# Optimization experiments

Measured on AMD Instinct MI355X. Metric: run time of the kernel, lower is better.

## Reference

```python
import jax, jax.numpy as jnp
import numpy as np

EPS = 1e-5       # InstanceNorm1d default eps
TEMP = 1.0       # temperature
SCALE = 8
# (name, arity) of the symbolic base, repeated SCALE times -> 48 functions, layer_size = 64
BASE = [("add", 2), ("mul", 2), ("sin", 1), ("cos", 1), ("tanh", 1), ("identity", 1)]


def _apply(name, a):
    if name == "add":
        return a[0] + a[1]
    if name == "mul":
        return a[0] * a[1]
    if name == "sin":
        return jnp.sin(a[0])
    if name == "cos":
        return jnp.cos(a[0])
    if name == "tanh":
        return jnp.tanh(a[0])
    return a[0]  # identity


def _inorm(x):
    # InstanceNorm1d, affine=False, biased variance, per (sample, channel) over L
    m = jnp.mean(x, axis=-1, keepdims=True)
    v = jnp.var(x, axis=-1, keepdims=True)
    return (x - m) * jax.lax.rsqrt(v + EPS)


def setup_inputs() -> dict:
    key = jax.random.key(0)
    k1, k2, k3 = jax.random.split(key, 3)
    x = jax.random.normal(k1, (64, 256, 4096), dtype=jnp.float32)
    w_channel = 0.1 * jax.random.normal(k2, (64, 256), dtype=jnp.float32)   # channel_conv 1x1
    w_down = 0.1 * jax.random.normal(k3, (48, 256), dtype=jnp.float32)      # down_conv 1x1
    return {"x": x, "w_channel": w_channel, "w_down": w_down}


def reference(x, w_channel, w_down):
    funcs = BASE * SCALE
    nx = _inorm(x)                                   # [B, C, L]
    # forward softmaxes channel_conv weight over output-channel dim (dim=0)
    w_eff = jax.nn.softmax(w_channel / TEMP, axis=0)  # [layer_size, C]
    multi = jnp.einsum("oc,bcl->bol", w_eff, nx)      # [B, layer_size, L]
    args_idx = 0
    output = None
    for i, (name, arity) in enumerate(funcs):
        args = [multi[:, args_idx + j : args_idx + j + 1] for j in range(arity)]
        img = _apply(name, args)                      # [B, 1, L]
        output = img if i == 0 else jnp.concatenate([output, img], axis=1)
        # original re-applies InstanceNorm to the growing tensor each iteration
        output = _inorm(output)
        args_idx += arity
    # skip connection
    output = output + jnp.einsum("oc,bcl->bol", w_down, nx)  # [B, 48, L]
    return output
```

## Files before the change

### kernel.cpp

```cpp
#include <hip/hip_runtime.h>
#include <hip/hip_bf16.h>

#define EPS 1e-5f

typedef unsigned int u32;
typedef unsigned short u16;
typedef __attribute__((ext_vector_type(8))) short bf16x8;
typedef __attribute__((ext_vector_type(4))) float f32x4;

__device__ __forceinline__ u32 f2bf(float f) {
    u32 u = __float_as_uint(f);
    u += 0x7FFFu + ((u >> 16) & 1u);
    return u >> 16;
}
__device__ __forceinline__ float bf2f(u32 h) {
    return __uint_as_float(h << 16);
}

__global__ __launch_bounds__(256) void k1_stats(const float* __restrict__ x,
                                                float* __restrict__ mean,
                                                float* __restrict__ rstd) {
    int row = blockIdx.x;
    const float* xr = x + (size_t)row * 4096;
    int t = threadIdx.x;
    float s = 0.f, ss = 0.f;
#pragma unroll
    for (int i = 0; i < 4; ++i) {
        float4 v = *(const float4*)(xr + t * 4 + i * 1024);
        s  += v.x + v.y + v.z + v.w;
        ss += v.x * v.x + v.y * v.y + v.z * v.z + v.w * v.w;
    }
    for (int off = 32; off > 0; off >>= 1) {
        s  += __shfl_down(s, off, 64);
        ss += __shfl_down(ss, off, 64);
    }
    __shared__ float red[8];
    int wid = t >> 6, lane = t & 63;
    if (lane == 0) { red[wid * 2] = s; red[wid * 2 + 1] = ss; }
    __syncthreads();
    if (t == 0) {
        float S  = red[0] + red[2] + red[4] + red[6];
        float SS = red[1] + red[3] + red[5] + red[7];
        float m = S * (1.f / 4096.f);
        float v = fmaxf(SS * (1.f / 4096.f) - m * m, 0.f);
        mean[row] = m;
        rstd[row] = rsqrtf(v + EPS);
    }
}

__global__ __launch_bounds__(256) void k2_prep(const float* __restrict__ wch,
                                               const float* __restrict__ wdn,
                                               const float* __restrict__ mean,
                                               const float* __restrict__ rstd,
                                               u16* __restrict__ Wc,
                                               float* __restrict__ bias,
                                               float* __restrict__ gsum,
                                               float* __restrict__ gss) {
    int b = blockIdx.x, t = threadIdx.x;
    __shared__ float smx[256], sinv[256], ssc[256], smn[256];
    {
        int c = t;
        float mx = -1e30f;
        for (int o = 0; o < 64; ++o) mx = fmaxf(mx, wch[o * 256 + c]);
        float sum = 0.f;
        for (int o = 0; o < 64; ++o) sum += __expf(wch[o * 256 + c] - mx);
        smx[c] = mx; sinv[c] = 1.f / sum;
        ssc[c] = rstd[b * 256 + c];
        smn[c] = mean[b * 256 + c];
    }
    __syncthreads();

    int lane = t & 63, w = t >> 6;
    int sub = lane >> 5, li = lane & 31;
    int c8 = li * 8;
    u16* Wb = Wc + (size_t)b * 128 * 256;
#pragma unroll 4
    for (int j = 0; j < 16; ++j) {
        int r = j * 8 + w * 2 + sub;
        float p = 0.f;
        u32 packed[4];
#pragma unroll
        for (int e = 0; e < 4; ++e) {
            u32 lohi[2];
#pragma unroll
            for (int h = 0; h < 2; ++h) {
                int c = c8 + 2 * e + h;
                float wv;
                if (r < 64)       wv = __expf(wch[r * 256 + c] - smx[c]) * sinv[c];
                else if (r < 112) wv = wdn[(r - 64) * 256 + c];
                else              wv = 0.f;
                u32 hb = f2bf(wv * ssc[c]);
                lohi[h] = hb;
                p += bf2f(hb) * smn[c];
            }
            packed[e] = lohi[0] | (lohi[1] << 16);
        }
        *(uint4*)&Wb[r * 256 + c8] = *(uint4*)packed;
#pragma unroll
        for (int off = 1; off <= 16; off <<= 1) p += __shfl_xor(p, off, 64);
        if (li == 0) bias[b * 128 + r] = -p;
    }
    if (t < 48) { gsum[b * 48 + t] = 0.f; gss[b * 48 + t] = 0.f; }
}

#define LSTR 36
__global__ __launch_bounds__(256, 4) void k3_main(const float* __restrict__ x,
                                                  const u16* __restrict__ Wc,
                                                  const float* __restrict__ bias,
                                                  u16* __restrict__ imgw,
                                                  u16* __restrict__ skipw,
                                                  float* __restrict__ gsum,
                                                  float* __restrict__ gss) {
    int lt = blockIdx.x;
    int b  = blockIdx.y;
    int n0blk = lt * 128;
    int t = threadIdx.x;
    int w = t >> 6, u = t & 63;
    int lane16 = u & 15, q = u >> 4;
    int m0  = (w & 1) * 64;
    int n0w = (w >> 1) * 64;

    __shared__ u32 Wl[128 * LSTR];
    __shared__ u32 xTl[128 * LSTR];
    __shared__ float sbias[128];

    if (t < 128) sbias[t] = bias[b * 128 + t];

    f32x4 acc[4][4];
#pragma unroll
    for (int mt = 0; mt < 4; ++mt)
#pragma unroll
        for (int nt = 0; nt < 4; ++nt) acc[mt][nt] = (f32x4){0.f, 0.f, 0.f, 0.f};

    const float* xb = x + (size_t)b * 256 * 4096 + n0blk;
    const u16* Wb = Wc + (size_t)b * 128 * 256;

    for (int cc = 0; cc < 4; ++cc) {
        int c0 = cc * 64;
        if (cc) __syncthreads();
#pragma unroll
        for (int p = 0; p < 4; ++p) {
            int sl = t + 256 * p;
            int m = sl >> 3, kq = sl & 7;
            uint4 v = *(const uint4*)(Wb + m * 256 + c0 + 8 * kq);
            *(uint4*)&Wl[m * LSTR + 4 * kq] = v;
        }
#pragma unroll
        for (int p = 0; p < 4; ++p) {
            int sl = t + 256 * p;
            int kp = sl & 31, nqq = sl >> 5;
            const float* xr = xb + (size_t)(c0 + 2 * kp) * 4096 + 4 * nqq;
            float4 r0 = *(const float4*)xr;
            float4 r1 = *(const float4*)(xr + 4096);
            int base = (4 * nqq) * LSTR + kp;
            xTl[base]            = f2bf(r0.x) | (f2bf(r1.x) << 16);
            xTl[base + LSTR]     = f2bf(r0.y) | (f2bf(r1.y) << 16);
            xTl[base + 2 * LSTR] = f2bf(r0.z) | (f2bf(r1.z) << 16);
            xTl[base + 3 * LSTR] = f2bf(r0.w) | (f2bf(r1.w) << 16);
        }
        __syncthreads();
#pragma unroll
        for (int kk = 0; kk < 2; ++kk) {
            int kwo = kk * 16 + q * 4;
            bf16x8 af[4], bfr[4];
#pragma unroll
            for (int mt = 0; mt < 4; ++mt)
                af[mt] = *(bf16x8*)&Wl[(m0 + 16 * mt + lane16) * LSTR + kwo];
#pragma unroll
            for (int nt = 0; nt < 4; ++nt)
                bfr[nt] = *(bf16x8*)&xTl[(n0w + 16 * nt + lane16) * LSTR + kwo];
#pragma unroll
            for (int mt = 0; mt < 4; ++mt)
#pragma unroll
                for (int nt = 0; nt < 4; ++nt)
                    acc[mt][nt] = __builtin_amdgcn_mfma_f32_16x16x32_bf16(af[mt], bfr[nt], acc[mt][nt], 0, 0, 0);
        }
    }
    __syncthreads();

    int jb = b * 48;
    if (m0 == 0) {
        int g2 = q >> 1, qo = q & 1;
#pragma unroll
        for (int mt = 0; mt < 4; ++mt) {
            int g = 2 * mt + g2;
            int j0 = 6 * g + (qo ? 2 : 0);
            int cnt = qo ? 4 : 2;
            float b0 = sbias[16 * mt + 4 * q + 0];
            float b1 = sbias[16 * mt + 4 * q + 1];
            float b2 = sbias[16 * mt + 4 * q + 2];
            float b3 = sbias[16 * mt + 4 * q + 3];
            float sj[4] = {0.f, 0.f, 0.f, 0.f};
            float qj[4] = {0.f, 0.f, 0.f, 0.f};
#pragma unroll
            for (int nt = 0; nt < 4; ++nt) {
                f32x4 a = acc[mt][nt];
                float a0 = a[0] + b0, a1 = a[1] + b1, a2 = a[2] + b2, a3 = a[3] + b3;
                int n = n0blk + n0w + 16 * nt + lane16;
                float v[4];
                if (!qo) {
                    v[0] = a0 + a1;
                    v[1] = a2 * a3;
                    v[2] = 0.f; v[3] = 0.f;
                } else {
                    v[0] = __sinf(a0);
                    v[1] = __cosf(a1);
                    float e = __expf(-2.f * fabsf(a2));
                    v[2] = copysignf((1.f - e) / (1.f + e), a2);
                    v[3] = a3;
                }
                for (int i = 0; i < cnt; ++i) {
                    imgw[(size_t)(jb + j0 + i) * 4096 + n] = (u16)f2bf(v[i]);
                    sj[i] += v[i];
                    qj[i] += v[i] * v[i];
                }
            }
#pragma unroll
            for (int off = 1; off <= 8; off <<= 1) {
#pragma unroll
                for (int i = 0; i < 4; ++i) {
                    sj[i] += __shfl_xor(sj[i], off, 64);
                    qj[i] += __shfl_xor(qj[i], off, 64);
                }
            }
            if (lane16 == 0) {
                for (int i = 0; i < cnt; ++i) {
                    atomicAdd(&gsum[jb + j0 + i], sj[i]);
                    atomicAdd(&gss[jb + j0 + i],  qj[i]);
                }
            }
        }
    } else {
#pragma unroll
        for (int mt = 0; mt < 3; ++mt) {
            int j0 = 16 * mt + 4 * q;
            float b0 = sbias[64 + j0 + 0];
            float b1 = sbias[64 + j0 + 1];
            float b2 = sbias[64 + j0 + 2];
            float b3 = sbias[64 + j0 + 3];
#pragma unroll
            for (int nt = 0; nt < 4; ++nt) {
                f32x4 a = acc[mt][nt];
                int n = n0blk + n0w + 16 * nt + lane16;
                skipw[(size_t)(jb + j0 + 0) * 4096 + n] = (u16)f2bf(a[0] + b0);
                skipw[(size_t)(jb + j0 + 1) * 4096 + n] = (u16)f2bf(a[1] + b1);
                skipw[(size_t)(jb + j0 + 2) * 4096 + n] = (u16)f2bf(a[2] + b2);
                skipw[(size_t)(jb + j0 + 3) * 4096 + n] = (u16)f2bf(a[3] + b3);
            }
        }
    }
}

__global__ __launch_bounds__(256) void k4_final(const u16* __restrict__ imgw,
                                                const u16* __restrict__ skipw,
                                                const float* __restrict__ gsum,
                                                const float* __restrict__ gss,
                                                float* __restrict__ out) {
    int j = blockIdx.x, b = blockIdx.y;
    int bj = b * 48 + j;
    float m = gsum[bj] * (1.f / 4096.f);
    float v = fmaxf(gss[bj] * (1.f / 4096.f) - m * m, 0.f);
    float rs = rsqrtf(v + EPS);
    float g = 1.f;
    float vv = v / (v + EPS);
    for (int k = 0; k < 47 - j; ++k) {
        g *= rsqrtf(vv + EPS);
        vv = vv / (vv + EPS);
    }
    float sc = rs * g;
    const u16* ir = imgw  + (size_t)bj * 4096;
    const u16* sr = skipw + (size_t)bj * 4096;
    float* orow = out + (size_t)bj * 4096;
    int t = threadIdx.x;
#pragma unroll
    for (int i = 0; i < 2; ++i) {
        int idx = t * 8 + i * 2048;
        uint4 iv = *(const uint4*)(ir + idx);
        uint4 sv = *(const uint4*)(sr + idx);
        const u32* ih = (const u32*)&iv;
        const u32* sh = (const u32*)&sv;
        float o[8];
#pragma unroll
        for (int e = 0; e < 4; ++e) {
            float i_lo = bf2f(ih[e] & 0xFFFFu), i_hi = bf2f(ih[e] >> 16);
            float s_lo = bf2f(sh[e] & 0xFFFFu), s_hi = bf2f(sh[e] >> 16);
            o[2 * e]     = (i_lo - m) * sc + s_lo;
            o[2 * e + 1] = (i_hi - m) * sc + s_hi;
        }
        *(float4*)(orow + idx)     = make_float4(o[0], o[1], o[2], o[3]);
        *(float4*)(orow + idx + 4) = make_float4(o[4], o[5], o[6], o[7]);
    }
}

extern "C" void kernel_launch(void* const* d_in, const int* in_sizes, int n_in,
                              void* d_out, int out_size, void* d_ws, size_t ws_size,
                              hipStream_t stream) {
    const float* x   = (const float*)d_in[0];
    const float* wch = (const float*)d_in[1];
    const float* wdn = (const float*)d_in[2];
    float* out = (float*)d_out;

    float* mean  = (float*)d_ws;
    float* rstd  = mean + 16384;
    float* bias  = rstd + 16384;
    float* gsum  = bias + 64 * 128;
    float* gss   = gsum + 3072;
    u16*   Wc    = (u16*)(gss + 3072);
    u16*   imgw  = Wc + (size_t)64 * 128 * 256;
    u16*   skipw = imgw + (size_t)64 * 48 * 4096;

    k1_stats<<<dim3(16384), dim3(256), 0, stream>>>(x, mean, rstd);
    k2_prep<<<dim3(64), dim3(256), 0, stream>>>(wch, wdn, mean, rstd, Wc, bias, gsum, gss);
    k3_main<<<dim3(32, 64), dim3(256), 0, stream>>>(x, Wc, bias, imgw, skipw, gsum, gss);
    k4_final<<<dim3(48, 64), dim3(256), 0, stream>>>(imgw, skipw, gsum, gss, out);
}
```

Baseline: 504.7 us.

## Precompute transposed bf16 x during stats pass; GEMM reads swizzled bf16 tiles

The stats kernel now also converts x to bf16 and writes it transposed ([B, L, C]) to workspace, accumulating per-channel sums with atomics after a memset. The main GEMM kernel loads contiguous 16-byte bf16 chunks for both operands into XOR-swizzled LDS instead of reading fp32 x, converting and transposing it in the inner loop. This moves conversion work out of k3 and halves the bytes k3 reads for x. The cost is a 128 MB extra write plus read of the transposed copy, and stats now come from atomics.

```diff
diff --git a/kernel.cpp b/kernel.cpp
--- a/kernel.cpp
+++ b/kernel.cpp
@@ -17,41 +17,57 @@
     return __uint_as_float(h << 16);
 }
 
-__global__ __launch_bounds__(256) void k1_stats(const float* __restrict__ x,
-                                                float* __restrict__ mean,
-                                                float* __restrict__ rstd) {
-    int row = blockIdx.x;
-    const float* xr = x + (size_t)row * 4096;
-    int t = threadIdx.x;
+__global__ __launch_bounds__(256) void k1_tstats(const float* __restrict__ x,
+                                                 u16* __restrict__ xT,
+                                                 float* __restrict__ gS,
+                                                 float* __restrict__ gSS) {
+    int b  = blockIdx.y;
+    int c0 = (blockIdx.x & 7) * 32;
+    int l0 = (blockIdx.x >> 3) * 512;
+    int t  = threadIdx.x;
+    __shared__ __align__(16) u16 T[512 * 32];
+
+    int crow = t >> 3;
+    int f4b  = t & 7;
+    const float* xr = x + ((size_t)(b * 256 + c0 + crow)) * 4096 + l0;
+    int cb   = (2 * crow) & 15;
+    int slot = crow >> 3;
     float s = 0.f, ss = 0.f;
 #pragma unroll
-    for (int i = 0; i < 4; ++i) {
-        float4 v = *(const float4*)(xr + t * 4 + i * 1024);
+    for (int i = 0; i < 16; ++i) {
+        int f4 = f4b + 8 * i;
+        float4 v = *(const float4*)(xr + 4 * f4);
         s  += v.x + v.y + v.z + v.w;
         ss += v.x * v.x + v.y * v.y + v.z * v.z + v.w * v.w;
-    }
-    for (int off = 32; off > 0; off >>= 1) {
-        s  += __shfl_down(s, off, 64);
-        ss += __shfl_down(ss, off, 64);
-    }
-    __shared__ float red[8];
-    int wid = t >> 6, lane = t & 63;
-    if (lane == 0) { red[wid * 2] = s; red[wid * 2 + 1] = ss; }
+        char* base = (char*)T + f4 * 256 + (((slot ^ (f4 & 3)) << 4) | cb);
+        *(u16*)(base      ) = (u16)f2bf(v.x);
+        *(u16*)(base +  64) = (u16)f2bf(v.y);
+        *(u16*)(base + 128) = (u16)f2bf(v.z);
+        *(u16*)(base + 192) = (u16)f2bf(v.w);
+    }
+    s += __shfl_xor(s, 1, 64); ss += __shfl_xor(ss, 1, 64);
+    s += __shfl_xor(s, 2, 64); ss += __shfl_xor(ss, 2, 64);
+    s += __shfl_xor(s, 4, 64); ss += __shfl_xor(ss, 4, 64);
+    if ((t & 7) == 0) {
+        atomicAdd(&gS [b * 256 + c0 + crow], s);
+        atomicAdd(&gSS[b * 256 + c0 + crow], ss);
+    }
     __syncthreads();
-    if (t == 0) {
-        float S  = red[0] + red[2] + red[4] + red[6];
-        float SS = red[1] + red[3] + red[5] + red[7];
-        float m = S * (1.f / 4096.f);
-        float v = fmaxf(SS * (1.f / 4096.f) - m * m, 0.f);
-        mean[row] = m;
-        rstd[row] = rsqrtf(v + EPS);
+    u16* xrow = xT + ((size_t)b * 4096 + l0) * 256 + c0;
+    int sslot = t & 3;
+#pragma unroll
+    for (int k = 0; k < 8; ++k) {
+        int ll  = k * 64 + (t >> 2);
+        int key = (ll >> 2) & 3;
+        uint4 vv = *(const uint4*)((const char*)T + ll * 64 + ((sslot ^ key) << 4));
+        *(uint4*)(xrow + (size_t)ll * 256 + 8 * sslot) = vv;
     }
 }
 
 __global__ __launch_bounds__(256) void k2_prep(const float* __restrict__ wch,
                                                const float* __restrict__ wdn,
-                                               const float* __restrict__ mean,
-                                               const float* __restrict__ rstd,
+                                               const float* __restrict__ gS,
+                                               const float* __restrict__ gSS,
                                                u16* __restrict__ Wc,
                                                float* __restrict__ bias,
                                                float* __restrict__ gsum,
@@ -65,8 +81,11 @@
         float sum = 0.f;
         for (int o = 0; o < 64; ++o) sum += __expf(wch[o * 256 + c] - mx);
         smx[c] = mx; sinv[c] = 1.f / sum;
-        ssc[c] = rstd[b * 256 + c];
-        smn[c] = mean[b * 256 + c];
+        float S = gS[b * 256 + c], Q = gSS[b * 256 + c];
+        float m = S * (1.f / 4096.f);
+        float v = fmaxf(Q * (1.f / 4096.f) - m * m, 0.f);
+        ssc[c] = rsqrtf(v + EPS);
+        smn[c] = m;
     }
     __syncthreads();
 
@@ -103,8 +122,7 @@
     if (t < 48) { gsum[b * 48 + t] = 0.f; gss[b * 48 + t] = 0.f; }
 }
 
-#define LSTR 36
-__global__ __launch_bounds__(256, 4) void k3_main(const float* __restrict__ x,
+__global__ __launch_bounds__(256, 4) void k3_main(const u16* __restrict__ xT,
                                                   const u16* __restrict__ Wc,
                                                   const float* __restrict__ bias,
                                                   u16* __restrict__ imgw,
@@ -120,8 +138,8 @@
     int m0  = (w & 1) * 64;
     int n0w = (w >> 1) * 64;
 
-    __shared__ u32 Wl[128 * LSTR];
-    __shared__ u32 xTl[128 * LSTR];
+    __shared__ __align__(16) u16 Wl[128 * 64];
+    __shared__ __align__(16) u16 Xl[128 * 64];
     __shared__ float sbias[128];
 
     if (t < 128) sbias[t] = bias[b * 128 + t];
@@ -132,43 +150,36 @@
 #pragma unroll
         for (int nt = 0; nt < 4; ++nt) acc[mt][nt] = (f32x4){0.f, 0.f, 0.f, 0.f};
 
-    const float* xb = x + (size_t)b * 256 * 4096 + n0blk;
-    const u16* Wb = Wc + (size_t)b * 128 * 256;
+    const char* Wb = (const char*)(Wc + (size_t)b * 128 * 256);
+    const char* xb = (const char*)(xT + ((size_t)b * 4096 + n0blk) * 256);
+
+    int r0   = t >> 3;
+    int jb   = (t & 7) << 4;
+    int swz0 = jb ^ (((t >> 3) & 7) << 4);
+    int swz16 = (lane16 & 7) << 4;
 
     for (int cc = 0; cc < 4; ++cc) {
-        int c0 = cc * 64;
         if (cc) __syncthreads();
+        int c0b = cc << 7;
 #pragma unroll
         for (int p = 0; p < 4; ++p) {
-            int sl = t + 256 * p;
-            int m = sl >> 3, kq = sl & 7;
-            uint4 v = *(const uint4*)(Wb + m * 256 + c0 + 8 * kq);
-            *(uint4*)&Wl[m * LSTR + 4 * kq] = v;
-        }
-#pragma unroll
-        for (int p = 0; p < 4; ++p) {
-            int sl = t + 256 * p;
-            int kp = sl & 31, nqq = sl >> 5;
-            const float* xr = xb + (size_t)(c0 + 2 * kp) * 4096 + 4 * nqq;
-            float4 r0 = *(const float4*)xr;
-            float4 r1 = *(const float4*)(xr + 4096);
-            int base = (4 * nqq) * LSTR + kp;
-            xTl[base]            = f2bf(r0.x) | (f2bf(r1.x) << 16);
-            xTl[base + LSTR]     = f2bf(r0.y) | (f2bf(r1.y) << 16);
-            xTl[base + 2 * LSTR] = f2bf(r0.z) | (f2bf(r1.z) << 16);
-            xTl[base + 3 * LSTR] = f2bf(r0.w) | (f2bf(r1.w) << 16);
+            int r = r0 + 32 * p;
+            uint4 wv = *(const uint4*)(Wb + (size_t)r * 512 + c0b + jb);
+            uint4 xv = *(const uint4*)(xb + (size_t)r * 512 + c0b + jb);
+            *(uint4*)((char*)Wl + r * 128 + swz0) = wv;
+            *(uint4*)((char*)Xl + r * 128 + swz0) = xv;
         }
         __syncthreads();
 #pragma unroll
         for (int kk = 0; kk < 2; ++kk) {
-            int kwo = kk * 16 + q * 4;
+            int kob = (kk * 64 + q * 16) ^ swz16;
             bf16x8 af[4], bfr[4];
 #pragma unroll
             for (int mt = 0; mt < 4; ++mt)
-                af[mt] = *(bf16x8*)&Wl[(m0 + 16 * mt + lane16) * LSTR + kwo];
+                af[mt] = *(const bf16x8*)((const char*)Wl + (m0 + 16 * mt + lane16) * 128 + kob);
 #pragma unroll
             for (int nt = 0; nt < 4; ++nt)
-                bfr[nt] = *(bf16x8*)&xTl[(n0w + 16 * nt + lane16) * LSTR + kwo];
+                bfr[nt] = *(const bf16x8*)((const char*)Xl + (n0w + 16 * nt + lane16) * 128 + kob);
 #pragma unroll
             for (int mt = 0; mt < 4; ++mt)
 #pragma unroll
@@ -178,7 +189,7 @@
     }
     __syncthreads();
 
-    int jb = b * 48;
+    int jb48 = b * 48;
     if (m0 == 0) {
         int g2 = q >> 1, qo = q & 1;
 #pragma unroll
@@ -210,7 +221,7 @@
                     v[3] = a3;
                 }
                 for (int i = 0; i < cnt; ++i) {
-                    imgw[(size_t)(jb + j0 + i) * 4096 + n] = (u16)f2bf(v[i]);
+                    imgw[(size_t)(jb48 + j0 + i) * 4096 + n] = (u16)f2bf(v[i]);
                     sj[i] += v[i];
                     qj[i] += v[i] * v[i];
                 }
@@ -225,8 +236,8 @@
             }
             if (lane16 == 0) {
                 for (int i = 0; i < cnt; ++i) {
-                    atomicAdd(&gsum[jb + j0 + i], sj[i]);
-                    atomicAdd(&gss[jb + j0 + i],  qj[i]);
+                    atomicAdd(&gsum[jb48 + j0 + i], sj[i]);
+                    atomicAdd(&gss[jb48 + j0 + i],  qj[i]);
                 }
             }
         }
@@ -242,10 +253,10 @@
             for (int nt = 0; nt < 4; ++nt) {
                 f32x4 a = acc[mt][nt];
                 int n = n0blk + n0w + 16 * nt + lane16;
-                skipw[(size_t)(jb + j0 + 0) * 4096 + n] = (u16)f2bf(a[0] + b0);
-                skipw[(size_t)(jb + j0 + 1) * 4096 + n] = (u16)f2bf(a[1] + b1);
-                skipw[(size_t)(jb + j0 + 2) * 4096 + n] = (u16)f2bf(a[2] + b2);
-                skipw[(size_t)(jb + j0 + 3) * 4096 + n] = (u16)f2bf(a[3] + b3);
+                skipw[(size_t)(jb48 + j0 + 0) * 4096 + n] = (u16)f2bf(a[0] + b0);
+                skipw[(size_t)(jb48 + j0 + 1) * 4096 + n] = (u16)f2bf(a[1] + b1);
+                skipw[(size_t)(jb48 + j0 + 2) * 4096 + n] = (u16)f2bf(a[2] + b2);
+                skipw[(size_t)(jb48 + j0 + 3) * 4096 + n] = (u16)f2bf(a[3] + b3);
             }
         }
     }
@@ -300,17 +311,19 @@
     const float* wdn = (const float*)d_in[2];
     float* out = (float*)d_out;
 
-    float* mean  = (float*)d_ws;
-    float* rstd  = mean + 16384;
-    float* bias  = rstd + 16384;
+    float* gS    = (float*)d_ws;
+    float* gSS   = gS + 16384;
+    float* bias  = gSS + 16384;
     float* gsum  = bias + 64 * 128;
     float* gss   = gsum + 3072;
     u16*   Wc    = (u16*)(gss + 3072);
-    u16*   imgw  = Wc + (size_t)64 * 128 * 256;
+    u16*   xTw   = Wc + (size_t)64 * 128 * 256;
+    u16*   imgw  = xTw + (size_t)64 * 4096 * 256;
     u16*   skipw = imgw + (size_t)64 * 48 * 4096;
 
-    k1_stats<<<dim3(16384), dim3(256), 0, stream>>>(x, mean, rstd);
-    k2_prep<<<dim3(64), dim3(256), 0, stream>>>(wch, wdn, mean, rstd, Wc, bias, gsum, gss);
-    k3_main<<<dim3(32, 64), dim3(256), 0, stream>>>(x, Wc, bias, imgw, skipw, gsum, gss);
+    hipMemsetAsync(gS, 0, 2 * 16384 * sizeof(float), stream);
+    k1_tstats<<<dim3(64, 64), dim3(256), 0, stream>>>(x, xTw, gS, gSS);
+    k2_prep<<<dim3(64), dim3(256), 0, stream>>>(wch, wdn, gS, gSS, Wc, bias, gsum, gss);
+    k3_main<<<dim3(32, 64), dim3(256), 0, stream>>>(xTw, Wc, bias, imgw, skipw, gsum, gss);
     k4_final<<<dim3(48, 64), dim3(256), 0, stream>>>(imgw, skipw, gsum, gss, out);
 }
```

After: 517.1 us. +2.5%, slower.
